# Kernel optimization log

Hardware: AMD Instinct MI355X
Metric: run time of the kernel (lower is better)

## Reference

```python
import jax, jax.numpy as jnp
import numpy as np
import math

IN_DIM = 2048
OUT_DIM = 2048
BATCH = 4096
BN_EPS = 1e-5


def setup_inputs() -> dict:
    key = jax.random.key(0)
    ks = jax.random.split(key, 6)
    x = jax.random.normal(ks[0], (BATCH, IN_DIM), dtype=jnp.float32)
    # scale ~ N(1.0, 0.1), translate = 0
    scale = 1.0 + 0.1 * jax.random.normal(ks[1], (1, IN_DIM), dtype=jnp.float32)
    translate = jnp.zeros((1, IN_DIM), dtype=jnp.float32)
    # kaiming-normal-ish init for wave_weight (fan_in), orthogonal-ish for base_weight
    wave_weight = jax.random.normal(ks[2], (OUT_DIM, IN_DIM), dtype=jnp.float32) * np.sqrt(2.0 / IN_DIM)
    bw = jax.random.normal(ks[3], (OUT_DIM, IN_DIM), dtype=jnp.float32)
    q, _ = jnp.linalg.qr(bw.T)  # (IN_DIM, OUT_DIM) orthonormal columns
    base_weight = q.T.astype(jnp.float32)
    gamma = jnp.ones((OUT_DIM,), dtype=jnp.float32)
    beta = jnp.zeros((OUT_DIM,), dtype=jnp.float32)
    return {"x": x, "scale": scale, "translate": translate,
            "wave_weight": wave_weight, "base_weight": base_weight,
            "gamma": gamma, "beta": beta}


def reference(x, scale, translate, wave_weight, base_weight, gamma, beta):
    # Bio wavelet: pi^-1/4 * cos(3u) * exp(-0.5 u^2), u = (x - t) / clamp(s, 1e-3)
    u = (x - translate) / jnp.maximum(scale, 1e-3)            # (B, in)
    wavelet = (math.pi ** -0.25) * jnp.cos(3.0 * u) * jnp.exp(-0.5 * u * u)
    # einsum 'boi,oi->bo' with singleton o broadcast == plain matmul
    wave_out = jnp.einsum('bi,oi->bo', wavelet, wave_weight)  # (B, out)
    base_out = jnp.einsum('bi,oi->bo', x, base_weight)        # (B, out)
    y = wave_out + 0.3 * base_out
    # BatchNorm1d (training mode: batch statistics, biased variance)
    mean = jnp.mean(y, axis=0)
    var = jnp.mean(jnp.square(y - mean), axis=0)
    out = gamma * (y - mean) * jax.lax.rsqrt(var + BN_EPS) + beta
    # dropout treated as identity (deterministic reference)
    return out
```

## Files before the change

### kernel.cpp

```cpp
#include <hip/hip_runtime.h>
#include <stdint.h>

#define IN_DIM 2048
#define OUT_DIM 2048
#define BATCH 4096
#define KDIM (2 * IN_DIM)
#define KROWB (KDIM * 2)
#define BN_EPS 1e-5f

typedef __attribute__((ext_vector_type(8))) short bf16x8;
typedef __attribute__((ext_vector_type(16))) float f32x16;

__device__ __forceinline__ unsigned short f2bf(float f) {
  union { float f; unsigned u; } v; v.f = f;
  unsigned r = v.u + 0x7FFFu + ((v.u >> 16) & 1u);
  return (unsigned short)(r >> 16);
}

__global__ void prep_act(const float* __restrict__ x,
                         const float* __restrict__ scale,
                         const float* __restrict__ translate,
                         unsigned short* __restrict__ A) {
  int e = (blockIdx.x * 256 + threadIdx.x) * 4;
  int b = e / IN_DIM;
  int i = e % IN_DIM;
  float4 xv = *(const float4*)(x + e);
  float4 sv = *(const float4*)(scale + i);
  float4 tv = *(const float4*)(translate + i);
  const float c = 0.7511255444649425f;
  float u0 = (xv.x - tv.x) / fmaxf(sv.x, 1e-3f);
  float u1 = (xv.y - tv.y) / fmaxf(sv.y, 1e-3f);
  float u2 = (xv.z - tv.z) / fmaxf(sv.z, 1e-3f);
  float u3 = (xv.w - tv.w) / fmaxf(sv.w, 1e-3f);
  ushort4 wv, xb;
  wv.x = f2bf(c * __cosf(3.0f * u0) * __expf(-0.5f * u0 * u0));
  wv.y = f2bf(c * __cosf(3.0f * u1) * __expf(-0.5f * u1 * u1));
  wv.z = f2bf(c * __cosf(3.0f * u2) * __expf(-0.5f * u2 * u2));
  wv.w = f2bf(c * __cosf(3.0f * u3) * __expf(-0.5f * u3 * u3));
  xb.x = f2bf(xv.x); xb.y = f2bf(xv.y); xb.z = f2bf(xv.z); xb.w = f2bf(xv.w);
  *(ushort4*)(A + (size_t)b * KDIM + i) = wv;
  *(ushort4*)(A + (size_t)b * KDIM + IN_DIM + i) = xb;
}

__global__ void prep_w(const float* __restrict__ ww,
                       const float* __restrict__ bw,
                       unsigned short* __restrict__ W) {
  int e = (blockIdx.x * 256 + threadIdx.x) * 4;
  int o = e / IN_DIM;
  int k = e % IN_DIM;
  float4 a = *(const float4*)(ww + e);
  float4 b = *(const float4*)(bw + e);
  ushort4 wa, wb;
  wa.x = f2bf(a.x); wa.y = f2bf(a.y); wa.z = f2bf(a.z); wa.w = f2bf(a.w);
  wb.x = f2bf(0.3f * b.x); wb.y = f2bf(0.3f * b.y);
  wb.z = f2bf(0.3f * b.z); wb.w = f2bf(0.3f * b.w);
  *(ushort4*)(W + (size_t)o * KDIM + k) = wa;
  *(ushort4*)(W + (size_t)o * KDIM + IN_DIM + k) = wb;
}


#define GLDS(gp, lo) __builtin_amdgcn_global_load_lds( \
    (const __attribute__((address_space(1))) void*)(gp), \
    (__attribute__((address_space(3))) void*)(lds + (lo) + ldsw), 16, 0, 0)

#define STAGE(SS, ap_, bp_) do { \
  GLDS((ap_),                (SS) * 49152 + 0); \
  GLDS((ap_) +  32 * KROWB,  (SS) * 49152 + 4096); \
  GLDS((ap_) +  64 * KROWB,  (SS) * 49152 + 8192); \
  GLDS((ap_) +  96 * KROWB,  (SS) * 49152 + 12288); \
  GLDS((bp_),                (SS) * 49152 + 16384); \
  GLDS((bp_) +  32 * KROWB,  (SS) * 49152 + 20480); \
  GLDS((bp_) +  64 * KROWB,  (SS) * 49152 + 24576); \
  GLDS((bp_) +  96 * KROWB,  (SS) * 49152 + 28672); \
  GLDS((bp_) + 128 * KROWB,  (SS) * 49152 + 32768); \
  GLDS((bp_) + 160 * KROWB,  (SS) * 49152 + 36864); \
  GLDS((bp_) + 192 * KROWB,  (SS) * 49152 + 40960); \
  GLDS((bp_) + 224 * KROWB,  (SS) * 49152 + 45056); \
} while (0)

#define LD6(S, sxv) do { \
  af0 = *(const bf16x8*)(lds + (S) * 49152 + ard + (sxv)); \
  af1 = *(const bf16x8*)(lds + (S) * 49152 + ard + 4096 + (sxv)); \
  bq0 = *(const bf16x8*)(lds + (S) * 49152 + brd + (sxv)); \
  bq1 = *(const bf16x8*)(lds + (S) * 49152 + brd + 4096 + (sxv)); \
  bq2 = *(const bf16x8*)(lds + (S) * 49152 + brd + 8192 + (sxv)); \
  bq3 = *(const bf16x8*)(lds + (S) * 49152 + brd + 12288 + (sxv)); \
} while (0)

#define MM8() do { \
  acc[0][0] = __builtin_amdgcn_mfma_f32_32x32x16_bf16(af0, bq0, acc[0][0], 0, 0, 0); \
  acc[0][1] = __builtin_amdgcn_mfma_f32_32x32x16_bf16(af0, bq1, acc[0][1], 0, 0, 0); \
  acc[0][2] = __builtin_amdgcn_mfma_f32_32x32x16_bf16(af0, bq2, acc[0][2], 0, 0, 0); \
  acc[0][3] = __builtin_amdgcn_mfma_f32_32x32x16_bf16(af0, bq3, acc[0][3], 0, 0, 0); \
  acc[1][0] = __builtin_amdgcn_mfma_f32_32x32x16_bf16(af1, bq0, acc[1][0], 0, 0, 0); \
  acc[1][1] = __builtin_amdgcn_mfma_f32_32x32x16_bf16(af1, bq1, acc[1][1], 0, 0, 0); \
  acc[1][2] = __builtin_amdgcn_mfma_f32_32x32x16_bf16(af1, bq2, acc[1][2], 0, 0, 0); \
  acc[1][3] = __builtin_amdgcn_mfma_f32_32x32x16_bf16(af1, bq3, acc[1][3], 0, 0, 0); \
} while (0)

#define LGKM0() asm volatile("s_waitcnt lgkmcnt(0)" ::: "memory")
#define VMW12() asm volatile("s_waitcnt vmcnt(12)" ::: "memory")
#define VMW0()  asm volatile("s_waitcnt vmcnt(0)" ::: "memory")
#define NOW()   do { } while (0)
#define BAR()   do { asm volatile("" ::: "memory"); __builtin_amdgcn_s_barrier(); \
                     asm volatile("" ::: "memory"); } while (0)

#define KT(S, SS, ap_, bp_, DOST, TAILW) do { \
  LD6(S, sx0); \
  if (DOST) STAGE(SS, ap_, bp_); \
  MM8(); \
  LD6(S, sx1); MM8(); \
  LD6(S, sx2); MM8(); \
  LD6(S, sx3); MM8(); \
  LGKM0(); TAILW; BAR(); \
} while (0)

__global__ __launch_bounds__(256, 1) void gemm128x256(
    const unsigned short* __restrict__ A,
    const unsigned short* __restrict__ W,
    float* __restrict__ Y,
    float* __restrict__ sums, float* __restrict__ sqs) {
  __shared__ char lds[147456];
  const int tid = threadIdx.x;
  const int lane = tid & 63;
  const int wave = tid >> 6;
  const int wm = wave >> 1;
  const int wn = wave & 1;

  const int sw = ((blockIdx.x & 7) << 5) | (blockIdx.x >> 3);
  const int brow = (sw & 31) * 128;
  const int bcol = (sw >> 5) * 256;

  const int srow = tid >> 3;
  const int skslot = (tid & 7) ^ (srow & 7);
  const char* aP = (const char*)A + (size_t)(brow + srow) * KROWB + skslot * 16;
  const char* bP = (const char*)W + (size_t)(bcol + srow) * KROWB + skslot * 16;
  const int ldsw = wave * 1024;

  const int ard = (wm * 64 + (lane & 31)) * 128;
  const int brd = 16384 + (wn * 128 + (lane & 31)) * 128;
  const int sx0 = (((lane >> 5) + 0) ^ (lane & 7)) << 4;
  const int sx1 = (((lane >> 5) + 2) ^ (lane & 7)) << 4;
  const int sx2 = (((lane >> 5) + 4) ^ (lane & 7)) << 4;
  const int sx3 = (((lane >> 5) + 6) ^ (lane & 7)) << 4;

  f32x16 acc[2][4];
#pragma unroll
  for (int m = 0; m < 2; ++m)
#pragma unroll
    for (int n = 0; n < 4; ++n)
      acc[m][n] = (f32x16){0.f, 0.f, 0.f, 0.f, 0.f, 0.f, 0.f, 0.f,
                           0.f, 0.f, 0.f, 0.f, 0.f, 0.f, 0.f, 0.f};
  bf16x8 af0, af1, bq0, bq1, bq2, bq3;

  STAGE(0, aP, bP);
  STAGE(1, aP + 128, bP + 128);
  VMW12(); BAR();

  const char* aSp = aP + 256;
  const char* bSp = bP + 256;

  for (int tt = 0; tt < 60; tt += 3) {
    KT(0, 2, aSp,       bSp,       1, VMW12());
    KT(1, 0, aSp + 128, bSp + 128, 1, VMW12());
    KT(2, 1, aSp + 256, bSp + 256, 1, VMW12());
    aSp += 384; bSp += 384;
  }
  KT(0, 2, aSp,       bSp,       1, VMW12());
  KT(1, 0, aSp + 128, bSp + 128, 1, VMW12());
  KT(2, 0, aSp, bSp, 0, VMW0());
  KT(0, 0, aSp, bSp, 0, NOW());

  const int r0 = brow + wm * 64 + 4 * (lane >> 5);
  const int c0 = bcol + wn * 128 + (lane & 31);
#pragma unroll
  for (int mb = 0; mb < 2; ++mb)
#pragma unroll
    for (int nb = 0; nb < 4; ++nb)
#pragma unroll
      for (int reg = 0; reg < 16; ++reg)
        Y[(size_t)(r0 + mb * 32 + (reg & 3) + 8 * (reg >> 2)) * OUT_DIM +
          (c0 + nb * 32)] = acc[mb][nb][reg];

#pragma unroll
  for (int nb = 0; nb < 4; ++nb) {
    float s = 0.f, q = 0.f;
#pragma unroll
    for (int mb = 0; mb < 2; ++mb)
#pragma unroll
      for (int reg = 0; reg < 16; ++reg) {
        float v = acc[mb][nb][reg];
        s += v; q += v * v;
      }
    s += __shfl_xor(s, 32); q += __shfl_xor(q, 32);
    if (lane < 32) {
      atomicAdd(&sums[c0 + nb * 32], s);
      atomicAdd(&sqs[c0 + nb * 32], q);
    }
  }
}

__global__ void bnorm(float* __restrict__ Y,
                      const float* __restrict__ sums, const float* __restrict__ sqs,
                      const float* __restrict__ gamma, const float* __restrict__ beta) {
  int e = (blockIdx.x * 256 + threadIdx.x) * 4;
  int c = e % OUT_DIM;
  float4 y = *(float4*)(Y + e);
  float4 s = *(const float4*)(sums + c);
  float4 q = *(const float4*)(sqs + c);
  float4 g = *(const float4*)(gamma + c);
  float4 bb = *(const float4*)(beta + c);
  const float invB = 1.0f / (float)BATCH;
  float m0 = s.x * invB, m1 = s.y * invB, m2 = s.z * invB, m3 = s.w * invB;
  float i0 = rsqrtf(q.x * invB - m0 * m0 + BN_EPS);
  float i1 = rsqrtf(q.y * invB - m1 * m1 + BN_EPS);
  float i2 = rsqrtf(q.z * invB - m2 * m2 + BN_EPS);
  float i3 = rsqrtf(q.w * invB - m3 * m3 + BN_EPS);
  y.x = g.x * (y.x - m0) * i0 + bb.x;
  y.y = g.y * (y.y - m1) * i1 + bb.y;
  y.z = g.z * (y.z - m2) * i2 + bb.z;
  y.w = g.w * (y.w - m3) * i3 + bb.w;
  *(float4*)(Y + e) = y;
}

extern "C" void kernel_launch(void* const* d_in, const int* in_sizes, int n_in,
                              void* d_out, int out_size, void* d_ws, size_t ws_size,
                              hipStream_t stream) {
  const float* x         = (const float*)d_in[0];
  const float* scale     = (const float*)d_in[1];
  const float* translate = (const float*)d_in[2];
  const float* ww        = (const float*)d_in[3];
  const float* bw        = (const float*)d_in[4];
  const float* gamma     = (const float*)d_in[5];
  const float* beta      = (const float*)d_in[6];
  float* out = (float*)d_out;

  char* ws = (char*)d_ws;
  unsigned short* A = (unsigned short*)ws;
  unsigned short* W = (unsigned short*)(ws + 33554432);
  float* sums = (float*)(ws + 50331648);
  float* sqs  = sums + OUT_DIM;

  hipMemsetAsync(sums, 0, 2 * OUT_DIM * sizeof(float), stream);
  prep_act<<<(BATCH * IN_DIM) / 1024, 256, 0, stream>>>(x, scale, translate, A);
  prep_w<<<(OUT_DIM * IN_DIM) / 1024, 256, 0, stream>>>(ww, bw, W);
  gemm128x256<<<256, 256, 0, stream>>>(A, W, out, sums, sqs);
  bnorm<<<(BATCH * OUT_DIM) / 1024, 256, 0, stream>>>(out, sums, sqs, gamma, beta);
}
```

Measured before the change: 114.5 us.

## Retile GEMM to 256x128 blocks with K=32 stages and two blocks per CU

Switches the fused GEMM tile from 128x256 to 256x128 and shrinks each K stage from 64 to 32 elements, cutting LDS use to 72KB so two blocks can fit per CU (launch_bounds 256,2). The LDS swizzle and the per-wave fragment layout are rebuilt for the 64-byte rows, and the MFMA groups are wrapped in s_setprio to favour matrix issue. The intent is better latency hiding through occupancy. The cost is twice as many barriers and pipeline stages per K, and the accumulators are capped by the two-blocks register limit. The grid stays at 256 blocks, so with 256 CUs the second block slot may never be filled.

```diff
diff --git a/kernel.cpp b/kernel.cpp
--- a/kernel.cpp
+++ b/kernel.cpp
@@ -63,64 +63,60 @@
     (const __attribute__((address_space(1))) void*)(gp), \
     (__attribute__((address_space(3))) void*)(lds + (lo) + ldsw), 16, 0, 0)
 
-#define STAGE(SS, ap_, bp_) do { \
-  GLDS((ap_),                (SS) * 49152 + 0); \
-  GLDS((ap_) +  32 * KROWB,  (SS) * 49152 + 4096); \
-  GLDS((ap_) +  64 * KROWB,  (SS) * 49152 + 8192); \
-  GLDS((ap_) +  96 * KROWB,  (SS) * 49152 + 12288); \
-  GLDS((bp_),                (SS) * 49152 + 16384); \
-  GLDS((bp_) +  32 * KROWB,  (SS) * 49152 + 20480); \
-  GLDS((bp_) +  64 * KROWB,  (SS) * 49152 + 24576); \
-  GLDS((bp_) +  96 * KROWB,  (SS) * 49152 + 28672); \
-  GLDS((bp_) + 128 * KROWB,  (SS) * 49152 + 32768); \
-  GLDS((bp_) + 160 * KROWB,  (SS) * 49152 + 36864); \
-  GLDS((bp_) + 192 * KROWB,  (SS) * 49152 + 40960); \
-  GLDS((bp_) + 224 * KROWB,  (SS) * 49152 + 45056); \
-} while (0)
-
-#define LD6(S, sxv) do { \
-  af0 = *(const bf16x8*)(lds + (S) * 49152 + ard + (sxv)); \
-  af1 = *(const bf16x8*)(lds + (S) * 49152 + ard + 4096 + (sxv)); \
-  bq0 = *(const bf16x8*)(lds + (S) * 49152 + brd + (sxv)); \
-  bq1 = *(const bf16x8*)(lds + (S) * 49152 + brd + 4096 + (sxv)); \
-  bq2 = *(const bf16x8*)(lds + (S) * 49152 + brd + 8192 + (sxv)); \
-  bq3 = *(const bf16x8*)(lds + (S) * 49152 + brd + 12288 + (sxv)); \
+#define STAGE(SS, OFS) do { \
+  GLDS(aPb + (OFS),               (SS) * 24576 + 0); \
+  GLDS(aPb + (OFS) +  64 * KROWB, (SS) * 24576 + 4096); \
+  GLDS(aPb + (OFS) + 128 * KROWB, (SS) * 24576 + 8192); \
+  GLDS(aPb + (OFS) + 192 * KROWB, (SS) * 24576 + 12288); \
+  GLDS(bPb + (OFS),               (SS) * 24576 + 16384); \
+  GLDS(bPb + (OFS) +  64 * KROWB, (SS) * 24576 + 20480); \
 } while (0)
 
 #define MM8() do { \
+  __builtin_amdgcn_s_setprio(1); \
   acc[0][0] = __builtin_amdgcn_mfma_f32_32x32x16_bf16(af0, bq0, acc[0][0], 0, 0, 0); \
   acc[0][1] = __builtin_amdgcn_mfma_f32_32x32x16_bf16(af0, bq1, acc[0][1], 0, 0, 0); \
-  acc[0][2] = __builtin_amdgcn_mfma_f32_32x32x16_bf16(af0, bq2, acc[0][2], 0, 0, 0); \
-  acc[0][3] = __builtin_amdgcn_mfma_f32_32x32x16_bf16(af0, bq3, acc[0][3], 0, 0, 0); \
   acc[1][0] = __builtin_amdgcn_mfma_f32_32x32x16_bf16(af1, bq0, acc[1][0], 0, 0, 0); \
   acc[1][1] = __builtin_amdgcn_mfma_f32_32x32x16_bf16(af1, bq1, acc[1][1], 0, 0, 0); \
-  acc[1][2] = __builtin_amdgcn_mfma_f32_32x32x16_bf16(af1, bq2, acc[1][2], 0, 0, 0); \
-  acc[1][3] = __builtin_amdgcn_mfma_f32_32x32x16_bf16(af1, bq3, acc[1][3], 0, 0, 0); \
+  acc[2][0] = __builtin_amdgcn_mfma_f32_32x32x16_bf16(af2, bq0, acc[2][0], 0, 0, 0); \
+  acc[2][1] = __builtin_amdgcn_mfma_f32_32x32x16_bf16(af2, bq1, acc[2][1], 0, 0, 0); \
+  acc[3][0] = __builtin_amdgcn_mfma_f32_32x32x16_bf16(af3, bq0, acc[3][0], 0, 0, 0); \
+  acc[3][1] = __builtin_amdgcn_mfma_f32_32x32x16_bf16(af3, bq1, acc[3][1], 0, 0, 0); \
+  __builtin_amdgcn_s_setprio(0); \
+} while (0)
+
+#define LD6(S, sxv) do { \
+  const char* Lb_ = lds + (S) * 24576; \
+  af0 = *(const bf16x8*)(Lb_ + aoff + 0 * 2048 + (sxv)); \
+  af1 = *(const bf16x8*)(Lb_ + aoff + 1 * 2048 + (sxv)); \
+  af2 = *(const bf16x8*)(Lb_ + aoff + 2 * 2048 + (sxv)); \
+  af3 = *(const bf16x8*)(Lb_ + aoff + 3 * 2048 + (sxv)); \
+  bq0 = *(const bf16x8*)(Lb_ + boff + 0 * 2048 + (sxv)); \
+  bq1 = *(const bf16x8*)(Lb_ + boff + 1 * 2048 + (sxv)); \
 } while (0)
 
 #define LGKM0() asm volatile("s_waitcnt lgkmcnt(0)" ::: "memory")
-#define VMW12() asm volatile("s_waitcnt vmcnt(12)" ::: "memory")
+#define VMW6()  asm volatile("s_waitcnt vmcnt(6)" ::: "memory")
 #define VMW0()  asm volatile("s_waitcnt vmcnt(0)" ::: "memory")
 #define NOW()   do { } while (0)
 #define BAR()   do { asm volatile("" ::: "memory"); __builtin_amdgcn_s_barrier(); \
                      asm volatile("" ::: "memory"); } while (0)
 
-#define KT(S, SS, ap_, bp_, DOST, TAILW) do { \
+#define KT(S, SS, SOFS, DOST, TAILW) do { \
   LD6(S, sx0); \
-  if (DOST) STAGE(SS, ap_, bp_); \
+  if (DOST) STAGE(SS, SOFS); \
   MM8(); \
-  LD6(S, sx1); MM8(); \
-  LD6(S, sx2); MM8(); \
-  LD6(S, sx3); MM8(); \
+  LD6(S, sx1); \
+  MM8(); \
   LGKM0(); TAILW; BAR(); \
 } while (0)
 
-__global__ __launch_bounds__(256, 1) void gemm128x256(
+__global__ __launch_bounds__(256, 2) void gemm256x128(
     const unsigned short* __restrict__ A,
     const unsigned short* __restrict__ W,
     float* __restrict__ Y,
     float* __restrict__ sums, float* __restrict__ sqs) {
-  __shared__ char lds[147456];
+  __shared__ char lds[73728];
   const int tid = threadIdx.x;
   const int lane = tid & 63;
   const int wave = tid >> 6;
@@ -128,74 +124,68 @@
   const int wn = wave & 1;
 
   const int sw = ((blockIdx.x & 7) << 5) | (blockIdx.x >> 3);
-  const int brow = (sw & 31) * 128;
-  const int bcol = (sw >> 5) * 256;
-
-  const int srow = tid >> 3;
-  const int skslot = (tid & 7) ^ (srow & 7);
-  const char* aP = (const char*)A + (size_t)(brow + srow) * KROWB + skslot * 16;
-  const char* bP = (const char*)W + (size_t)(bcol + srow) * KROWB + skslot * 16;
+  const int brow = (sw & 15) * 256;
+  const int bcol = (sw >> 4) * 128;
+
+  const int srow = tid >> 2;
+  const int sksl = (tid & 3) ^ ((tid >> 3) & 3);
+  const char* aPb = (const char*)A + (size_t)(brow + srow) * KROWB + sksl * 16;
+  const char* bPb = (const char*)W + (size_t)(bcol + srow) * KROWB + sksl * 16;
   const int ldsw = wave * 1024;
 
-  const int ard = (wm * 64 + (lane & 31)) * 128;
-  const int brd = 16384 + (wn * 128 + (lane & 31)) * 128;
-  const int sx0 = (((lane >> 5) + 0) ^ (lane & 7)) << 4;
-  const int sx1 = (((lane >> 5) + 2) ^ (lane & 7)) << 4;
-  const int sx2 = (((lane >> 5) + 4) ^ (lane & 7)) << 4;
-  const int sx3 = (((lane >> 5) + 6) ^ (lane & 7)) << 4;
-
-  f32x16 acc[2][4];
-#pragma unroll
-  for (int m = 0; m < 2; ++m)
-#pragma unroll
-    for (int n = 0; n < 4; ++n)
+  const int lx = lane & 31;
+  const int xorv = (lx >> 1) & 3;
+  const int aoff = (wm * 128 + lx) * 64;
+  const int boff = 16384 + (wn * 64 + lx) * 64;
+  const int sx0 = ((((lane >> 5))     ^ xorv) << 4);
+  const int sx1 = ((((lane >> 5) + 2) ^ xorv) << 4);
+
+  f32x16 acc[4][2];
+#pragma unroll
+  for (int m = 0; m < 4; ++m)
+#pragma unroll
+    for (int n = 0; n < 2; ++n)
       acc[m][n] = (f32x16){0.f, 0.f, 0.f, 0.f, 0.f, 0.f, 0.f, 0.f,
                            0.f, 0.f, 0.f, 0.f, 0.f, 0.f, 0.f, 0.f};
-  bf16x8 af0, af1, bq0, bq1, bq2, bq3;
-
-  STAGE(0, aP, bP);
-  STAGE(1, aP + 128, bP + 128);
-  VMW12(); BAR();
-
-  const char* aSp = aP + 256;
-  const char* bSp = bP + 256;
-
-  for (int tt = 0; tt < 60; tt += 3) {
-    KT(0, 2, aSp,       bSp,       1, VMW12());
-    KT(1, 0, aSp + 128, bSp + 128, 1, VMW12());
-    KT(2, 1, aSp + 256, bSp + 256, 1, VMW12());
-    aSp += 384; bSp += 384;
+  bf16x8 af0, af1, af2, af3, bq0, bq1;
+
+  STAGE(0, 0);
+  STAGE(1, 64);
+  VMW6(); BAR();
+
+  for (int tb = 0; tb < 126; tb += 3) {
+    KT(0, 2, (tb + 2) * 64, 1, VMW6());
+    KT(1, 0, (tb + 3) * 64, 1, VMW6());
+    KT(2, 1, (tb + 4) * 64, 1, VMW6());
   }
-  KT(0, 2, aSp,       bSp,       1, VMW12());
-  KT(1, 0, aSp + 128, bSp + 128, 1, VMW12());
-  KT(2, 0, aSp, bSp, 0, VMW0());
-  KT(0, 0, aSp, bSp, 0, NOW());
-
-  const int r0 = brow + wm * 64 + 4 * (lane >> 5);
-  const int c0 = bcol + wn * 128 + (lane & 31);
-#pragma unroll
-  for (int mb = 0; mb < 2; ++mb)
-#pragma unroll
-    for (int nb = 0; nb < 4; ++nb)
+  KT(0, 0, 0, 0, VMW0());
+  KT(1, 0, 0, 0, NOW());
+
+  const int r0 = brow + wm * 128 + 4 * (lane >> 5);
+  const int c0 = bcol + wn * 64 + lx;
+#pragma unroll
+  for (int mf = 0; mf < 4; ++mf)
+#pragma unroll
+    for (int nf = 0; nf < 2; ++nf)
 #pragma unroll
       for (int reg = 0; reg < 16; ++reg)
-        Y[(size_t)(r0 + mb * 32 + (reg & 3) + 8 * (reg >> 2)) * OUT_DIM +
-          (c0 + nb * 32)] = acc[mb][nb][reg];
-
-#pragma unroll
-  for (int nb = 0; nb < 4; ++nb) {
+        Y[(size_t)(r0 + mf * 32 + (reg & 3) + 8 * (reg >> 2)) * OUT_DIM +
+          (c0 + nf * 32)] = acc[mf][nf][reg];
+
+#pragma unroll
+  for (int nf = 0; nf < 2; ++nf) {
     float s = 0.f, q = 0.f;
 #pragma unroll
-    for (int mb = 0; mb < 2; ++mb)
+    for (int mf = 0; mf < 4; ++mf)
 #pragma unroll
       for (int reg = 0; reg < 16; ++reg) {
-        float v = acc[mb][nb][reg];
+        float v = acc[mf][nf][reg];
         s += v; q += v * v;
       }
     s += __shfl_xor(s, 32); q += __shfl_xor(q, 32);
     if (lane < 32) {
-      atomicAdd(&sums[c0 + nb * 32], s);
-      atomicAdd(&sqs[c0 + nb * 32], q);
+      atomicAdd(&sums[c0 + nf * 32], s);
+      atomicAdd(&sqs[c0 + nf * 32], q);
     }
   }
 }
@@ -244,6 +234,6 @@
   hipMemsetAsync(sums, 0, 2 * OUT_DIM * sizeof(float), stream);
   prep_act<<<(BATCH * IN_DIM) / 1024, 256, 0, stream>>>(x, scale, translate, A);
   prep_w<<<(OUT_DIM * IN_DIM) / 1024, 256, 0, stream>>>(ww, bw, W);
-  gemm128x256<<<256, 256, 0, stream>>>(A, W, out, sums, sqs);
+  gemm256x128<<<256, 256, 0, stream>>>(A, W, out, sums, sqs);
   bnorm<<<(BATCH * OUT_DIM) / 1024, 256, 0, stream>>>(out, sums, sqs, gamma, beta);
 }
```

Measured after the change: 117.1 us. 2.3% more time.
